# Kernel optimization log

Hardware: AMD Instinct MI355X
Metric: run time of the kernel (lower is better)

The kernel has to match this reference:

```python
import jax, jax.numpy as jnp
import numpy as np

B, N, C = 2, 2048, 1024
H = 16
R = 4
MLP = 4096
LORA_SCALE = 1.0 / R  # lora_alpha=1, r=4
EPS = 1e-5


def _ln(x, g, b):
    m = jnp.mean(x, axis=-1, keepdims=True)
    v = jnp.mean(jnp.square(x - m), axis=-1, keepdims=True)
    return (x - m) * jax.lax.rsqrt(v + EPS) * g + b


def setup_inputs() -> dict:
    key = jax.random.key(0)
    ks = jax.random.split(key, 16)
    s = lambda k, shape, fan: jax.random.normal(k, shape, jnp.float32) * (1.0 / np.sqrt(fan))
    return {
        "x": jax.random.normal(ks[0], (B, N, C), jnp.float32),
        "pos": jax.random.normal(ks[1], (B, N, C), jnp.float32),
        "Wqkv": s(ks[2], (3 * C, C), C),
        "b_qkv": jnp.zeros((3 * C,), jnp.float32),
        "lora_A": s(ks[3], (2 * R, C), C),          # rows 0:R -> q, R:2R -> v
        "lora_B": s(ks[4], (2 * C, R), R) * 0.1,     # rows 0:C -> q, C:2C -> v
        "Wproj": s(ks[5], (C, C), C),
        "b_proj": jnp.zeros((C,), jnp.float32),
        "ln1_g": jnp.ones((C,), jnp.float32),
        "ln1_b": jnp.zeros((C,), jnp.float32),
        "ln2_g": jnp.ones((C,), jnp.float32),
        "ln2_b": jnp.zeros((C,), jnp.float32),
        "W1": s(ks[6], (MLP, C), C),
        "b1": jnp.zeros((MLP,), jnp.float32),
        "W2": s(ks[7], (C, MLP), MLP),
        "b2": jnp.zeros((C,), jnp.float32),
        "idx": 0,
    }


def reference(x, pos, Wqkv, b_qkv, lora_A, lora_B, Wproj, b_proj,
              ln1_g, ln1_b, ln2_g, ln2_b, W1, b1, W2, b2, idx):
    # (dropout layers are identity in eval mode)
    x = x + pos

    # --- attention block: Residual(PreNormDrop(SelfAttention)) ---
    h = _ln(x, ln1_g, ln1_b)                              # [B,N,C]
    qkv = h @ Wqkv.T + b_qkv                              # [B,N,3C]
    # LoRA MergedLinear: low-rank update on q and v thirds only
    after_A = h @ lora_A.T                                # [B,N,2R]
    dq = after_A[..., :R] @ lora_B[:C].T * LORA_SCALE     # [B,N,C]
    dv = after_A[..., R:] @ lora_B[C:].T * LORA_SCALE     # [B,N,C]
    qkv = qkv.at[..., :C].add(dq).at[..., 2 * C:].add(dv)

    Dh = C // H
    q, k, v = [t.reshape(B, N, H, Dh).transpose(0, 2, 1, 3)
               for t in jnp.split(qkv, 3, axis=-1)]       # each [B,H,N,Dh]
    scale = Dh ** -0.5
    attn = jnp.einsum('bhid,bhjd->bhij', q, k) * scale    # [B,H,N,N]
    attn = jax.nn.softmax(attn, axis=-1)
    o = jnp.einsum('bhij,bhjd->bhid', attn, v)            # [B,H,N,Dh]
    o = o.transpose(0, 2, 1, 3).reshape(B, N, C)
    o = o @ Wproj.T + b_proj
    x = x + o

    # --- FFN block: Residual(PreNorm(FeedForward)) ---
    h2 = _ln(x, ln2_g, ln2_b)
    h2 = jax.nn.gelu(h2 @ W1.T + b1, approximate=False)
    h2 = h2 @ W2.T + b2
    return x + h2
```

## Files before the change

### kernel.cpp

```cpp
#include <hip/hip_runtime.h>
#include <hip/hip_bf16.h>
#include <math.h>

typedef __hip_bfloat16 bf16;
typedef __attribute__((ext_vector_type(4))) float f32x4;
typedef __attribute__((ext_vector_type(16))) float f32x16;
typedef __attribute__((ext_vector_type(8))) short s16x8;

__device__ __forceinline__ void async_cp16(void* lds, const void* g) {
    __builtin_amdgcn_global_load_lds((const __attribute__((address_space(1))) void*)g,
                                     (__attribute__((address_space(3))) void*)lds, 16, 0, 0);
}

__device__ __forceinline__ float gelu_fast(float x) {
    float y = 1.5957691216f * (x + 0.044715f * x * x * x);
    float t = __expf(y);
    float th = 1.0f - 2.0f / (t + 1.0f);
    return 0.5f * x * (1.0f + th);
}

__global__ __launch_bounds__(256)
void cvt_all(const float* __restrict__ w0, const float* __restrict__ w1,
             const float* __restrict__ w2, const float* __restrict__ w3,
             bf16* __restrict__ o0, bf16* __restrict__ o1,
             bf16* __restrict__ o2, bf16* __restrict__ o3) {
    int i = blockIdx.x * 256 + threadIdx.x;
    const float* src; bf16* dst; int j = i;
    if (j < 786432)            { src = w0; dst = o0; }
    else if (j < 1048576)      { j -= 786432;  src = w1; dst = o1; }
    else if (j < 2097152)      { j -= 1048576; src = w2; dst = o2; }
    else                       { j -= 2097152; src = w3; dst = o3; }
    float4 v = ((const float4*)src)[j];
    union { bf16 o[4]; uint2 u; } pk;
    pk.o[0] = __float2bfloat16(v.x); pk.o[1] = __float2bfloat16(v.y);
    pk.o[2] = __float2bfloat16(v.z); pk.o[3] = __float2bfloat16(v.w);
    ((uint2*)dst)[j] = pk.u;
}

template <bool ADD>
__global__ __launch_bounds__(256)
void ln_kernel(const float* __restrict__ xin, const float* __restrict__ pos,
               const float* __restrict__ gam, const float* __restrict__ bet,
               float* __restrict__ x1, bf16* __restrict__ hout) {
    const int row = blockIdx.x, tid = threadIdx.x;
    const size_t off = (size_t)row * 1024;
    float4 v = ((const float4*)(xin + off))[tid];
    if constexpr (ADD) {
        float4 p = ((const float4*)(pos + off))[tid];
        v.x += p.x; v.y += p.y; v.z += p.z; v.w += p.w;
        ((float4*)(x1 + off))[tid] = v;
    }
    float s  = v.x + v.y + v.z + v.w;
    float s2 = v.x*v.x + v.y*v.y + v.z*v.z + v.w*v.w;
#pragma unroll
    for (int o = 32; o >= 1; o >>= 1) { s += __shfl_xor(s, o); s2 += __shfl_xor(s2, o); }
    __shared__ float sS[4], sS2[4];
    int w = tid >> 6, lane = tid & 63;
    if (lane == 0) { sS[w] = s; sS2[w] = s2; }
    __syncthreads();
    float mean = (sS[0] + sS[1] + sS[2] + sS[3]) * (1.f / 1024.f);
    float e2   = (sS2[0] + sS2[1] + sS2[2] + sS2[3]) * (1.f / 1024.f);
    float rstd = rsqrtf(e2 - mean * mean + 1e-5f);
    float4 gv = ((const float4*)gam)[tid], bv = ((const float4*)bet)[tid];
    bf16* ho = hout + off + tid * 4;
    ho[0] = __float2bfloat16((v.x - mean) * rstd * gv.x + bv.x);
    ho[1] = __float2bfloat16((v.y - mean) * rstd * gv.y + bv.y);
    ho[2] = __float2bfloat16((v.z - mean) * rstd * gv.z + bv.z);
    ho[3] = __float2bfloat16((v.w - mean) * rstd * gv.w + bv.w);
}

template <int MODE>
__global__ __launch_bounds__(512)
void gemm_bk64(const bf16* __restrict__ A, const bf16* __restrict__ B,
               const float* __restrict__ bias, bf16* __restrict__ outp,
               int M, int N, int K, int gx) {
    __shared__ bf16 As[3][256 * 64];
    __shared__ bf16 Bs[3][128 * 64];
    const int tid = threadIdx.x;
    const int lane = tid & 63, w = tid >> 6;
    const int grp = lane >> 4, c16 = lane & 15;
    const int wm = (w & 3) * 64, wn = (w >> 2) * 64;
    const int nwg = gridDim.x, bid = blockIdx.x;
    const int sw = (bid & 7) * (nwg >> 3) + (bid >> 3);
    const int bm = (sw / gx) * 256, bn = (sw % gx) * 128;

    f32x4 acc[4][4];
    const f32x4 zero = {0.f, 0.f, 0.f, 0.f};
#pragma unroll
    for (int mi = 0; mi < 4; mi++)
#pragma unroll
        for (int ni = 0; ni < 4; ni++) acc[mi][ni] = zero;

#define STAGE128(bufi, k0)                                                          \
    {                                                                               \
        const int buf_ = (bufi);                                                    \
        const int koff_ = (k0);                                                     \
        _Pragma("unroll") for (int t_ = 0; t_ < 4; t_++) {                          \
            int s_ = t_ * 512 + tid;                                                \
            int row_ = s_ >> 3, db_ = s_ & 7;                                       \
            int gb_ = (db_ ^ (row_ & 7)) << 3;                                      \
            async_cp16(&As[buf_][s_ * 8], A + (size_t)(bm + row_) * K + koff_ + gb_); \
        }                                                                           \
        _Pragma("unroll") for (int t_ = 0; t_ < 2; t_++) {                          \
            int s_ = t_ * 512 + tid;                                                \
            int row_ = s_ >> 3, db_ = s_ & 7;                                       \
            int gb_ = (db_ ^ (row_ & 7)) << 3;                                      \
            async_cp16(&Bs[buf_][s_ * 8], B + (size_t)(bn + row_) * K + koff_ + gb_); \
        }                                                                           \
    }

#define COMPUTE128(bufi)                                                            \
    {                                                                               \
        const int buf_ = (bufi);                                                    \
        _Pragma("unroll") for (int kc_ = 0; kc_ < 2; kc_++) {                       \
            s16x8 af_[4], bfv_[4];                                                  \
            _Pragma("unroll") for (int mi_ = 0; mi_ < 4; mi_++) {                   \
                int r_ = wm + mi_ * 16 + c16;                                       \
                af_[mi_] = *(const s16x8*)&As[buf_][r_ * 64 + ((((kc_ << 2) | grp) ^ (r_ & 7)) << 3)]; \
            }                                                                       \
            _Pragma("unroll") for (int ni_ = 0; ni_ < 4; ni_++) {                   \
                int r_ = wn + ni_ * 16 + c16;                                       \
                bfv_[ni_] = *(const s16x8*)&Bs[buf_][r_ * 64 + ((((kc_ << 2) | grp) ^ (r_ & 7)) << 3)]; \
            }                                                                       \
            _Pragma("unroll") for (int mi_ = 0; mi_ < 4; mi_++)                     \
                _Pragma("unroll") for (int ni_ = 0; ni_ < 4; ni_++)                 \
                    acc[mi_][ni_] = __builtin_amdgcn_mfma_f32_16x16x32_bf16(af_[mi_], bfv_[ni_], acc[mi_][ni_], 0, 0, 0); \
        }                                                                           \
    }

#define WAITV12 asm volatile("s_waitcnt vmcnt(12)" ::: "memory")
#define WAITV6  asm volatile("s_waitcnt vmcnt(6)"  ::: "memory")
#define WAITV0  asm volatile("s_waitcnt vmcnt(0)"  ::: "memory")

#define STEP128(BQ, TQ)                                                             \
    {                                                                               \
        const int tq_ = (TQ);                                                       \
        COMPUTE128(BQ);                                                             \
        __builtin_amdgcn_s_barrier();            \
        if (tq_ + 3 < nk) { STAGE128(BQ, (tq_ + 3) << 6); WAITV12; }                 \
        else if (tq_ + 2 < nk) { WAITV6; }                                          \
        else { WAITV0; }                                \
        __builtin_amdgcn_s_barrier();             \
    }

    const int nk = K >> 6;
    STAGE128(0, 0);
    STAGE128(1, 64);
    STAGE128(2, 128);
    WAITV12;
    __builtin_amdgcn_s_barrier();

    for (int t = 0; t < nk - 1; t += 3) {
        STEP128(0, t);
        STEP128(1, t + 1);
        STEP128(2, t + 2);
    }
    COMPUTE128(0);

#undef STEP128
#undef WAITV12
#undef WAITV6
#undef WAITV0
#undef STAGE128
#undef COMPUTE128

#pragma unroll
    for (int mi = 0; mi < 4; mi++)
#pragma unroll
        for (int ni = 0; ni < 4; ni++) {
            int r0 = bm + wm + mi * 16 + grp * 4;
            int c  = bn + wn + ni * 16 + c16;
            float bv = bias[c];
#pragma unroll
            for (int q = 0; q < 4; q++) {
                size_t idx = (size_t)(r0 + q) * N + c;
                float v = acc[mi][ni][q] + bv;
                if constexpr (MODE == 2) v = gelu_fast(v);
                outp[idx] = __float2bfloat16(v);
            }
        }
}

__global__ __launch_bounds__(256)
void gemm_n64(const bf16* __restrict__ A, const bf16* __restrict__ B,
              const float* __restrict__ bias, const float* __restrict__ resid,
              float* __restrict__ outp, int M, int N, int K, int gx) {
    __shared__ bf16 As[3][128 * 64];
    __shared__ bf16 Bs[3][64 * 64];
    const int tid = threadIdx.x;
    const int lane = tid & 63, w = tid >> 6;
    const int grp = lane >> 4, c16 = lane & 15;
    const int wm = w * 32;
    const int nwg = gridDim.x, bid = blockIdx.x;
    const int sw = (bid & 7) * (nwg >> 3) + (bid >> 3);
    const int bm = (sw / gx) * 128, bn = (sw % gx) * 64;

    f32x4 acc[2][4];
    const f32x4 zero = {0.f, 0.f, 0.f, 0.f};
#pragma unroll
    for (int mi = 0; mi < 2; mi++)
#pragma unroll
        for (int ni = 0; ni < 4; ni++) acc[mi][ni] = zero;

#define STAGE64(bufi, k0)                                                           \
    {                                                                               \
        const int buf_ = (bufi);                                                    \
        const int koff_ = (k0);                                                     \
        _Pragma("unroll") for (int t_ = 0; t_ < 4; t_++) {                          \
            int s_ = t_ * 256 + tid;                                                \
            int row_ = s_ >> 3, db_ = s_ & 7;                                       \
            async_cp16(&As[buf_][s_ * 8], A + (size_t)(bm + row_) * K + koff_ + ((db_ ^ (row_ & 7)) << 3)); \
        }                                                                           \
        _Pragma("unroll") for (int t_ = 0; t_ < 2; t_++) {                          \
            int s_ = t_ * 256 + tid;                                                \
            int row_ = s_ >> 3, db_ = s_ & 7;                                       \
            async_cp16(&Bs[buf_][s_ * 8], B + (size_t)(bn + row_) * K + koff_ + ((db_ ^ (row_ & 7)) << 3)); \
        }                                                                           \
    }

#define COMPUTE64(bufi)                                                             \
    {                                                                               \
        const int buf_ = (bufi);                                                    \
        _Pragma("unroll") for (int kc_ = 0; kc_ < 2; kc_++) {                       \
            s16x8 af_[2], bfv_[4];                                                  \
            _Pragma("unroll") for (int mi_ = 0; mi_ < 2; mi_++) {                   \
                int r_ = wm + mi_ * 16 + c16;                                       \
                af_[mi_] = *(const s16x8*)&As[buf_][r_ * 64 + ((((kc_ << 2) | grp) ^ (r_ & 7)) << 3)]; \
            }                                                                       \
            _Pragma("unroll") for (int ni_ = 0; ni_ < 4; ni_++) {                   \
                int rb_ = ni_ * 16 + c16;                                           \
                bfv_[ni_] = *(const s16x8*)&Bs[buf_][rb_ * 64 + ((((kc_ << 2) | grp) ^ (rb_ & 7)) << 3)]; \
            }                                                                       \
            _Pragma("unroll") for (int mi_ = 0; mi_ < 2; mi_++)                     \
                _Pragma("unroll") for (int ni_ = 0; ni_ < 4; ni_++)                 \
                    acc[mi_][ni_] = __builtin_amdgcn_mfma_f32_16x16x32_bf16(af_[mi_], bfv_[ni_], acc[mi_][ni_], 0, 0, 0); \
        }                                                                           \
    }

#define WAITV12 asm volatile("s_waitcnt vmcnt(12)" ::: "memory")
#define WAITV6  asm volatile("s_waitcnt vmcnt(6)"  ::: "memory")
#define WAITV0  asm volatile("s_waitcnt vmcnt(0)"  ::: "memory")

#define STEP64(BQ, TQ)                                                              \
    {                                                                               \
        const int tq_ = (TQ);                                                       \
        COMPUTE64(BQ);                                                              \
        __builtin_amdgcn_s_barrier();            \
        if (tq_ + 3 < nk) { STAGE64(BQ, (tq_ + 3) << 6); WAITV12; }                 \
        else if (tq_ + 2 < nk) { WAITV6; }                                          \
        else { WAITV0; }                                \
        __builtin_amdgcn_s_barrier();             \
    }

    const int nk = K >> 6;
    STAGE64(0, 0);
    STAGE64(1, 64);
    STAGE64(2, 128);
    WAITV12;
    __builtin_amdgcn_s_barrier();

    for (int t = 0; t < nk - 1; t += 3) {
        STEP64(0, t);
        STEP64(1, t + 1);
        STEP64(2, t + 2);
    }
    COMPUTE64(0);

#undef STEP64
#undef WAITV12
#undef WAITV6
#undef WAITV0
#undef STAGE64
#undef COMPUTE64

#pragma unroll
    for (int mi = 0; mi < 2; mi++)
#pragma unroll
        for (int ni = 0; ni < 4; ni++) {
            int r0 = bm + wm + mi * 16 + grp * 4;
            int c  = bn + ni * 16 + c16;
            float bv = bias[c];
#pragma unroll
            for (int q = 0; q < 4; q++) {
                size_t idx = (size_t)(r0 + q) * N + c;
                outp[idx] = acc[mi][ni][q] + bv + resid[idx];
            }
        }
}

__global__ __launch_bounds__(256)
void lora_a_kernel(const bf16* __restrict__ h, const float* __restrict__ A,
                   float* __restrict__ afterA) {
    const int row = blockIdx.x, tid = threadIdx.x;
    float hv[4];
#pragma unroll
    for (int t = 0; t < 4; t++) hv[t] = __bfloat162float(h[(size_t)row * 1024 + tid * 4 + t]);
    float p[8];
#pragma unroll
    for (int r = 0; r < 8; r++) {
        float4 av = ((const float4*)(A + (size_t)r * 1024))[tid];
        p[r] = hv[0] * av.x + hv[1] * av.y + hv[2] * av.z + hv[3] * av.w;
    }
#pragma unroll
    for (int r = 0; r < 8; r++)
#pragma unroll
        for (int o = 32; o >= 1; o >>= 1) p[r] += __shfl_xor(p[r], o);
    __shared__ float red[4][8];
    int w = tid >> 6, lane = tid & 63;
    if (lane == 0) {
#pragma unroll
        for (int r = 0; r < 8; r++) red[w][r] = p[r];
    }
    __syncthreads();
    if (tid < 8) afterA[(size_t)row * 8 + tid] = red[0][tid] + red[1][tid] + red[2][tid] + red[3][tid];
}

__global__ __launch_bounds__(256)
void attn_prep(const bf16* __restrict__ qkv, const float* __restrict__ afterA,
               const float* __restrict__ loraB, bf16* __restrict__ Qb,
               bf16* __restrict__ Kb, bf16* __restrict__ Vt) {
    const int bh = blockIdx.y, b = bh >> 4, h = bh & 15;
    const int it = blockIdx.x;
    __shared__ bf16 Vs[64 * 65];
    const int tid = threadIdx.x;
#pragma unroll
    for (int t = 0; t < 16; t++) {
        int s = t * 256 + tid;
        int il = s >> 6, d = s & 63;
        int ig = b * 2048 + it * 64 + il;
        size_t grow = (size_t)ig * 3072 + h * 64 + d;
        int col = h * 64 + d;
        const float* aA = afterA + (size_t)ig * 8;
        float4 bq = ((const float4*)loraB)[col];
        float4 bvv = ((const float4*)loraB)[1024 + col];
        float dq = (aA[0]*bq.x  + aA[1]*bq.y  + aA[2]*bq.z  + aA[3]*bq.w)  * 0.25f;
        float dv = (aA[4]*bvv.x + aA[5]*bvv.y + aA[6]*bvv.z + aA[7]*bvv.w) * 0.25f;
        float q = (__bfloat162float(qkv[grow]) + dq) * 0.18033688011f;
        float k = __bfloat162float(qkv[grow + 1024]);
        float v = __bfloat162float(qkv[grow + 2048]) + dv;
        size_t orow = (size_t)(bh * 2048 + it * 64 + il) * 64 + d;
        Qb[orow] = __float2bfloat16(q);
        Kb[orow] = __float2bfloat16(k);
        Vs[d * 65 + il] = __float2bfloat16(v);
    }
    __syncthreads();
#pragma unroll
    for (int t = 0; t < 16; t++) {
        int s = t * 256 + tid;
        int d = s >> 6, il = s & 63;
        Vt[(size_t)(bh * 64 + d) * 2048 + it * 64 + il] = Vs[d * 65 + il];
    }
}

__global__ __launch_bounds__(256)
void attn_fused(const bf16* __restrict__ Qb, const bf16* __restrict__ Kb,
                const bf16* __restrict__ Vt, bf16* __restrict__ Og) {
    __shared__ bf16 Qs[128 * 64], Ks[2][64 * 64], Vs[2][64 * 64];
    const int tid = threadIdx.x;
    const int lane = tid & 63, w = tid >> 6;
    const int c32 = lane & 31, l5 = lane >> 5;
    const int bid = blockIdx.x;
    const int sw = (bid & 7) * 64 + (bid >> 3);
    const int bh = sw >> 4, b = bh >> 4, h = bh & 15;
    const int i0 = (sw & 15) * 128;
    const int rowperm = (c32 & 19) | (((c32 >> 3) & 1) << 2) | (((c32 >> 2) & 1) << 3);

    const size_t qbase = (size_t)(bh * 2048 + i0) * 64;
    const size_t kbase = (size_t)bh * 2048 * 64;
    const size_t vbase = (size_t)bh * 64 * 2048;

#define STAGEKV(bufi, jv)                                                           \
    {                                                                               \
        const int buf_ = (bufi);                                                    \
        const int joff_ = (jv);                                                     \
        _Pragma("unroll") for (int t_ = 0; t_ < 2; t_++) {                          \
            int s_ = t_ * 256 + tid;                                                \
            int row_ = s_ >> 3, db_ = s_ & 7;                                       \
            int gb_ = (db_ ^ (row_ & 7)) << 3;                                      \
            async_cp16(&Ks[buf_][s_ * 8], Kb + kbase + (size_t)(joff_ + row_) * 64 + gb_); \
            async_cp16(&Vs[buf_][s_ * 8], Vt + vbase + (size_t)row_ * 2048 + joff_ + gb_); \
        }                                                                           \
    }

#pragma unroll
    for (int t = 0; t < 4; t++) {
        int s = t * 256 + tid;
        int row = s >> 3, db = s & 7;
        async_cp16(&Qs[s * 8], Qb + qbase + row * 64 + ((db ^ (row & 7)) << 3));
    }
    STAGEKV(0, 0);
    __syncthreads();

    s16x8 qf[4];
    {
        int rq = w * 32 + c32;
#pragma unroll
        for (int kc = 0; kc < 4; kc++) {
            int db = 2 * kc + l5;
            qf[kc] = *(const s16x8*)&Qs[rq * 64 + ((db ^ (rq & 7)) << 3)];
        }
    }

    f32x16 Oq[2];
#pragma unroll
    for (int dq = 0; dq < 2; dq++)
#pragma unroll
        for (int r = 0; r < 16; r++) Oq[dq][r] = 0.f;
    float l_lane = 0.f;

#define ATILE(BUF, JN)                                                              \
    {                                                                               \
        const int jn_ = (JN);                                                       \
        if (jn_ < 32) { STAGEKV((BUF) ^ 1, jn_ << 6); }                             \
        f32x16 Sq[2];                                                               \
        __builtin_amdgcn_s_setprio(1);                                              \
        _Pragma("unroll") for (int jq_ = 0; jq_ < 2; jq_++) {                       \
            _Pragma("unroll") for (int r_ = 0; r_ < 16; r_++) Sq[jq_][r_] = 0.f;    \
            int rk_ = jq_ * 32 + rowperm;                                           \
            _Pragma("unroll") for (int kc_ = 0; kc_ < 4; kc_++) {                   \
                int db_ = 2 * kc_ + l5;                                             \
                s16x8 af_ = *(const s16x8*)&Ks[BUF][rk_ * 64 + ((db_ ^ (rk_ & 7)) << 3)]; \
                Sq[jq_] = __builtin_amdgcn_mfma_f32_32x32x16_bf16(af_, qf[kc_], Sq[jq_], 0, 0, 0); \
            }                                                                       \
        }                                                                           \
        __builtin_amdgcn_s_setprio(0);                                              \
        s16x8 pf_[4];                                                               \
        _Pragma("unroll") for (int kc_ = 0; kc_ < 4; kc_++) {                       \
            union { s16x8 v; unsigned u4[4]; } u_;                                  \
            _Pragma("unroll") for (int pr_ = 0; pr_ < 4; pr_++) {                   \
                float a_ = Sq[kc_ >> 1][8 * (kc_ & 1) + 2 * pr_];                   \
                float b_ = Sq[kc_ >> 1][8 * (kc_ & 1) + 2 * pr_ + 1];               \
                float pa_, pb_;                                                     \
                asm("v_exp_f32 %0, %1" : "=v"(pa_) : "v"(a_));                      \
                asm("v_exp_f32 %0, %1" : "=v"(pb_) : "v"(b_));                      \
                l_lane += pa_; l_lane += pb_;                                       \
                unsigned pk_;                                                       \
                asm("v_cvt_pk_bf16_f32 %0, %1, %2" : "=v"(pk_) : "v"(pa_), "v"(pb_)); \
                u_.u4[pr_] = pk_;                                                   \
            }                                                                       \
            pf_[kc_] = u_.v;                                                        \
        }                                                                           \
        __builtin_amdgcn_s_setprio(1);                                              \
        _Pragma("unroll") for (int dq_ = 0; dq_ < 2; dq_++) {                       \
            int rd_ = dq_ * 32 + c32;                                               \
            _Pragma("unroll") for (int kc_ = 0; kc_ < 4; kc_++) {                   \
                int jb_ = 2 * kc_ + l5;                                             \
                s16x8 af_ = *(const s16x8*)&Vs[BUF][rd_ * 64 + ((jb_ ^ (rd_ & 7)) << 3)]; \
                Oq[dq_] = __builtin_amdgcn_mfma_f32_32x32x16_bf16(af_, pf_[kc_], Oq[dq_], 0, 0, 0); \
            }                                                                       \
        }                                                                           \
        __builtin_amdgcn_s_setprio(0);                                              \
        __syncthreads();                                                            \
    }

    for (int jt = 0; jt < 32; jt += 2) {
        ATILE(0, jt + 1);
        ATILE(1, jt + 2);
    }
#undef ATILE
#undef STAGEKV

    float l = l_lane + __shfl_xor(l_lane, 32);
    float inv = 1.0f / fmaxf(l, 1e-35f);
    int i = i0 + w * 32 + c32;
    size_t obase = (size_t)(b * 2048 + i) * 1024 + h * 64;
#pragma unroll
    for (int dq = 0; dq < 2; dq++)
#pragma unroll
        for (int rg = 0; rg < 4; rg++) {
            union { bf16 e[4]; uint2 u; } pk;
#pragma unroll
            for (int c = 0; c < 4; c++)
                pk.e[c] = __float2bfloat16(Oq[dq][rg * 4 + c] * inv);
            int d0 = dq * 32 + l5 * 4 + rg * 8;
            *(uint2*)&Og[obase + d0] = pk.u;
        }
}

extern "C" void kernel_launch(void* const* d_in, const int* in_sizes, int n_in,
                              void* d_out, int out_size, void* d_ws, size_t ws_size,
                              hipStream_t stream) {
    const float* x     = (const float*)d_in[0];
    const float* pos   = (const float*)d_in[1];
    const float* Wqkv  = (const float*)d_in[2];
    const float* bqkv  = (const float*)d_in[3];
    const float* loraA = (const float*)d_in[4];
    const float* loraB = (const float*)d_in[5];
    const float* Wproj = (const float*)d_in[6];
    const float* bproj = (const float*)d_in[7];
    const float* ln1g  = (const float*)d_in[8];
    const float* ln1b  = (const float*)d_in[9];
    const float* ln2g  = (const float*)d_in[10];
    const float* ln2b  = (const float*)d_in[11];
    const float* W1    = (const float*)d_in[12];
    const float* b1    = (const float*)d_in[13];
    const float* W2    = (const float*)d_in[14];
    const float* b2    = (const float*)d_in[15];

    char* ws = (char*)d_ws;
    float* x1     = (float*)(ws + 0);
    bf16*  hbuf   = (bf16*) (ws + 16777216);
    bf16*  qkv    = (bf16*) (ws + 25165824);
    bf16*  gbuf   = (bf16*) (ws + 50331648);
    float* afterA = (float*)(ws + 83886080);
    bf16*  Qb     = (bf16*) (ws + 84017152);
    bf16*  Kb     = (bf16*) (ws + 92405760);
    bf16*  Vt     = (bf16*) (ws + 100794368);
    bf16*  Obf    = (bf16*) (ws + 109182976);
    bf16*  Wqkvb  = (bf16*) (ws + 117571584);
    bf16*  Wprojb = (bf16*) (ws + 123863040);
    bf16*  W1b    = (bf16*) (ws + 125960192);
    bf16*  W2b    = (bf16*) (ws + 134348800);

    cvt_all<<<12288, 256, 0, stream>>>(Wqkv, Wproj, W1, W2, Wqkvb, Wprojb, W1b, W2b);

    ln_kernel<true><<<4096, 256, 0, stream>>>(x, pos, ln1g, ln1b, x1, hbuf);

    gemm_bk64<0><<<384, 512, 0, stream>>>(hbuf, Wqkvb, bqkv, qkv, 4096, 3072, 1024, 24);

    lora_a_kernel<<<4096, 256, 0, stream>>>(hbuf, loraA, afterA);

    attn_prep<<<dim3(32, 32), 256, 0, stream>>>(qkv, afterA, loraB, Qb, Kb, Vt);
    attn_fused<<<512, 256, 0, stream>>>(Qb, Kb, Vt, Obf);

    gemm_n64<<<512, 256, 0, stream>>>(Obf, Wprojb, bproj, x1, x1, 4096, 1024, 1024, 16);

    ln_kernel<false><<<4096, 256, 0, stream>>>(x1, nullptr, ln2g, ln2b, nullptr, hbuf);

    gemm_bk64<2><<<512, 512, 0, stream>>>(hbuf, W1b, b1, gbuf, 4096, 4096, 1024, 32);

    gemm_n64<<<512, 256, 0, stream>>>(gbuf, W2b, b2, x1, (float*)d_out, 4096, 1024, 4096, 16);

    (void)in_sizes; (void)n_in; (void)out_size; (void)ws_size;
}
```

Before: 381.7 us.

## Enlarge per-warp GEMM tiles and halve threads per block

The 256x128 GEMM now runs with 4 warps instead of 8, so each warp computes a 128x64 sub-tile with 32 accumulators. The N=1024 GEMMs move from 128x64 to 128x128 block tiles, with each warp computing 64x64. Both changes raise MFMA work per LDS fragment load and cut block count. The cost is higher register pressure, fewer waves per CU for latency hiding, and for the N=1024 GEMMs only 256 blocks, which may underfill the CUs.

```diff
diff --git a/kernel.cpp b/kernel.cpp
--- a/kernel.cpp
+++ b/kernel.cpp
@@ -70,7 +70,7 @@
 }
 
 template <int MODE>
-__global__ __launch_bounds__(512)
+__global__ __launch_bounds__(256, 1)
 void gemm_bk64(const bf16* __restrict__ A, const bf16* __restrict__ B,
                const float* __restrict__ bias, bf16* __restrict__ outp,
                int M, int N, int K, int gx) {
@@ -79,15 +79,15 @@
     const int tid = threadIdx.x;
     const int lane = tid & 63, w = tid >> 6;
     const int grp = lane >> 4, c16 = lane & 15;
-    const int wm = (w & 3) * 64, wn = (w >> 2) * 64;
+    const int wm = (w & 1) * 128, wn = (w >> 1) * 64;
     const int nwg = gridDim.x, bid = blockIdx.x;
     const int sw = (bid & 7) * (nwg >> 3) + (bid >> 3);
     const int bm = (sw / gx) * 256, bn = (sw % gx) * 128;
 
-    f32x4 acc[4][4];
+    f32x4 acc[8][4];
     const f32x4 zero = {0.f, 0.f, 0.f, 0.f};
 #pragma unroll
-    for (int mi = 0; mi < 4; mi++)
+    for (int mi = 0; mi < 8; mi++)
 #pragma unroll
         for (int ni = 0; ni < 4; ni++) acc[mi][ni] = zero;
 
@@ -95,14 +95,14 @@
     {                                                                               \
         const int buf_ = (bufi);                                                    \
         const int koff_ = (k0);                                                     \
-        _Pragma("unroll") for (int t_ = 0; t_ < 4; t_++) {                          \
-            int s_ = t_ * 512 + tid;                                                \
+        _Pragma("unroll") for (int t_ = 0; t_ < 8; t_++) {                          \
+            int s_ = t_ * 256 + tid;                                                \
             int row_ = s_ >> 3, db_ = s_ & 7;                                       \
             int gb_ = (db_ ^ (row_ & 7)) << 3;                                      \
             async_cp16(&As[buf_][s_ * 8], A + (size_t)(bm + row_) * K + koff_ + gb_); \
         }                                                                           \
-        _Pragma("unroll") for (int t_ = 0; t_ < 2; t_++) {                          \
-            int s_ = t_ * 512 + tid;                                                \
+        _Pragma("unroll") for (int t_ = 0; t_ < 4; t_++) {                          \
+            int s_ = t_ * 256 + tid;                                                \
             int row_ = s_ >> 3, db_ = s_ & 7;                                       \
             int gb_ = (db_ ^ (row_ & 7)) << 3;                                      \
             async_cp16(&Bs[buf_][s_ * 8], B + (size_t)(bn + row_) * K + koff_ + gb_); \
@@ -113,8 +113,8 @@
     {                                                                               \
         const int buf_ = (bufi);                                                    \
         _Pragma("unroll") for (int kc_ = 0; kc_ < 2; kc_++) {                       \
-            s16x8 af_[4], bfv_[4];                                                  \
-            _Pragma("unroll") for (int mi_ = 0; mi_ < 4; mi_++) {                   \
+            s16x8 af_[8], bfv_[4];                                                  \
+            _Pragma("unroll") for (int mi_ = 0; mi_ < 8; mi_++) {                   \
                 int r_ = wm + mi_ * 16 + c16;                                       \
                 af_[mi_] = *(const s16x8*)&As[buf_][r_ * 64 + ((((kc_ << 2) | grp) ^ (r_ & 7)) << 3)]; \
             }                                                                       \
@@ -122,14 +122,14 @@
                 int r_ = wn + ni_ * 16 + c16;                                       \
                 bfv_[ni_] = *(const s16x8*)&Bs[buf_][r_ * 64 + ((((kc_ << 2) | grp) ^ (r_ & 7)) << 3)]; \
             }                                                                       \
-            _Pragma("unroll") for (int mi_ = 0; mi_ < 4; mi_++)                     \
+            _Pragma("unroll") for (int mi_ = 0; mi_ < 8; mi_++)                     \
                 _Pragma("unroll") for (int ni_ = 0; ni_ < 4; ni_++)                 \
                     acc[mi_][ni_] = __builtin_amdgcn_mfma_f32_16x16x32_bf16(af_[mi_], bfv_[ni_], acc[mi_][ni_], 0, 0, 0); \
         }                                                                           \
     }
 
+#define WAITV24 asm volatile("s_waitcnt vmcnt(24)" ::: "memory")
 #define WAITV12 asm volatile("s_waitcnt vmcnt(12)" ::: "memory")
-#define WAITV6  asm volatile("s_waitcnt vmcnt(6)"  ::: "memory")
 #define WAITV0  asm volatile("s_waitcnt vmcnt(0)"  ::: "memory")
 
 #define STEP128(BQ, TQ)                                                             \
@@ -137,8 +137,8 @@
         const int tq_ = (TQ);                                                       \
         COMPUTE128(BQ);                                                             \
         __builtin_amdgcn_s_barrier();            \
-        if (tq_ + 3 < nk) { STAGE128(BQ, (tq_ + 3) << 6); WAITV12; }                 \
-        else if (tq_ + 2 < nk) { WAITV6; }                                          \
+        if (tq_ + 3 < nk) { STAGE128(BQ, (tq_ + 3) << 6); WAITV24; }                \
+        else if (tq_ + 2 < nk) { WAITV12; }                                         \
         else { WAITV0; }                                \
         __builtin_amdgcn_s_barrier();             \
     }
@@ -147,7 +147,7 @@
     STAGE128(0, 0);
     STAGE128(1, 64);
     STAGE128(2, 128);
-    WAITV12;
+    WAITV24;
     __builtin_amdgcn_s_barrier();
 
     for (int t = 0; t < nk - 1; t += 3) {
@@ -158,14 +158,14 @@
     COMPUTE128(0);
 
 #undef STEP128
+#undef WAITV24
 #undef WAITV12
-#undef WAITV6
 #undef WAITV0
 #undef STAGE128
 #undef COMPUTE128
 
 #pragma unroll
-    for (int mi = 0; mi < 4; mi++)
+    for (int mi = 0; mi < 8; mi++)
 #pragma unroll
         for (int ni = 0; ni < 4; ni++) {
             int r0 = bm + wm + mi * 16 + grp * 4;
@@ -181,24 +181,24 @@
         }
 }
 
-__global__ __launch_bounds__(256)
+__global__ __launch_bounds__(256, 1)
 void gemm_n64(const bf16* __restrict__ A, const bf16* __restrict__ B,
               const float* __restrict__ bias, const float* __restrict__ resid,
               float* __restrict__ outp, int M, int N, int K, int gx) {
     __shared__ bf16 As[3][128 * 64];
-    __shared__ bf16 Bs[3][64 * 64];
+    __shared__ bf16 Bs[3][128 * 64];
     const int tid = threadIdx.x;
     const int lane = tid & 63, w = tid >> 6;
     const int grp = lane >> 4, c16 = lane & 15;
-    const int wm = w * 32;
+    const int wm = (w & 1) * 64, wn = (w >> 1) * 64;
     const int nwg = gridDim.x, bid = blockIdx.x;
     const int sw = (bid & 7) * (nwg >> 3) + (bid >> 3);
-    const int bm = (sw / gx) * 128, bn = (sw % gx) * 64;
-
-    f32x4 acc[2][4];
+    const int bm = (sw / gx) * 128, bn = (sw % gx) * 128;
+
+    f32x4 acc[4][4];
     const f32x4 zero = {0.f, 0.f, 0.f, 0.f};
 #pragma unroll
-    for (int mi = 0; mi < 2; mi++)
+    for (int mi = 0; mi < 4; mi++)
 #pragma unroll
         for (int ni = 0; ni < 4; ni++) acc[mi][ni] = zero;
 
@@ -209,12 +209,9 @@
         _Pragma("unroll") for (int t_ = 0; t_ < 4; t_++) {                          \
             int s_ = t_ * 256 + tid;                                                \
             int row_ = s_ >> 3, db_ = s_ & 7;                                       \
-            async_cp16(&As[buf_][s_ * 8], A + (size_t)(bm + row_) * K + koff_ + ((db_ ^ (row_ & 7)) << 3)); \
-        }                                                                           \
-        _Pragma("unroll") for (int t_ = 0; t_ < 2; t_++) {                          \
-            int s_ = t_ * 256 + tid;                                                \
-            int row_ = s_ >> 3, db_ = s_ & 7;                                       \
-            async_cp16(&Bs[buf_][s_ * 8], B + (size_t)(bn + row_) * K + koff_ + ((db_ ^ (row_ & 7)) << 3)); \
+            int gb_ = (db_ ^ (row_ & 7)) << 3;                                      \
+            async_cp16(&As[buf_][s_ * 8], A + (size_t)(bm + row_) * K + koff_ + gb_); \
+            async_cp16(&Bs[buf_][s_ * 8], B + (size_t)(bn + row_) * K + koff_ + gb_); \
         }                                                                           \
     }
 
@@ -222,23 +219,23 @@
     {                                                                               \
         const int buf_ = (bufi);                                                    \
         _Pragma("unroll") for (int kc_ = 0; kc_ < 2; kc_++) {                       \
-            s16x8 af_[2], bfv_[4];                                                  \
-            _Pragma("unroll") for (int mi_ = 0; mi_ < 2; mi_++) {                   \
+            s16x8 af_[4], bfv_[4];                                                  \
+            _Pragma("unroll") for (int mi_ = 0; mi_ < 4; mi_++) {                   \
                 int r_ = wm + mi_ * 16 + c16;                                       \
                 af_[mi_] = *(const s16x8*)&As[buf_][r_ * 64 + ((((kc_ << 2) | grp) ^ (r_ & 7)) << 3)]; \
             }                                                                       \
             _Pragma("unroll") for (int ni_ = 0; ni_ < 4; ni_++) {                   \
-                int rb_ = ni_ * 16 + c16;                                           \
-                bfv_[ni_] = *(const s16x8*)&Bs[buf_][rb_ * 64 + ((((kc_ << 2) | grp) ^ (rb_ & 7)) << 3)]; \
-            }                                                                       \
-            _Pragma("unroll") for (int mi_ = 0; mi_ < 2; mi_++)                     \
+                int r_ = wn + ni_ * 16 + c16;                                       \
+                bfv_[ni_] = *(const s16x8*)&Bs[buf_][r_ * 64 + ((((kc_ << 2) | grp) ^ (r_ & 7)) << 3)]; \
+            }                                                                       \
+            _Pragma("unroll") for (int mi_ = 0; mi_ < 4; mi_++)                     \
                 _Pragma("unroll") for (int ni_ = 0; ni_ < 4; ni_++)                 \
                     acc[mi_][ni_] = __builtin_amdgcn_mfma_f32_16x16x32_bf16(af_[mi_], bfv_[ni_], acc[mi_][ni_], 0, 0, 0); \
         }                                                                           \
     }
 
-#define WAITV12 asm volatile("s_waitcnt vmcnt(12)" ::: "memory")
-#define WAITV6  asm volatile("s_waitcnt vmcnt(6)"  ::: "memory")
+#define WAITV16 asm volatile("s_waitcnt vmcnt(16)" ::: "memory")
+#define WAITV8  asm volatile("s_waitcnt vmcnt(8)"  ::: "memory")
 #define WAITV0  asm volatile("s_waitcnt vmcnt(0)"  ::: "memory")
 
 #define STEP64(BQ, TQ)                                                              \
@@ -246,8 +243,8 @@
         const int tq_ = (TQ);                                                       \
         COMPUTE64(BQ);                                                              \
         __builtin_amdgcn_s_barrier();            \
-        if (tq_ + 3 < nk) { STAGE64(BQ, (tq_ + 3) << 6); WAITV12; }                 \
-        else if (tq_ + 2 < nk) { WAITV6; }                                          \
+        if (tq_ + 3 < nk) { STAGE64(BQ, (tq_ + 3) << 6); WAITV16; }                 \
+        else if (tq_ + 2 < nk) { WAITV8; }                                          \
         else { WAITV0; }                                \
         __builtin_amdgcn_s_barrier();             \
     }
@@ -256,7 +253,7 @@
     STAGE64(0, 0);
     STAGE64(1, 64);
     STAGE64(2, 128);
-    WAITV12;
+    WAITV16;
     __builtin_amdgcn_s_barrier();
 
     for (int t = 0; t < nk - 1; t += 3) {
@@ -267,18 +264,18 @@
     COMPUTE64(0);
 
 #undef STEP64
-#undef WAITV12
-#undef WAITV6
+#undef WAITV16
+#undef WAITV8
 #undef WAITV0
 #undef STAGE64
 #undef COMPUTE64
 
 #pragma unroll
-    for (int mi = 0; mi < 2; mi++)
+    for (int mi = 0; mi < 4; mi++)
 #pragma unroll
         for (int ni = 0; ni < 4; ni++) {
             int r0 = bm + wm + mi * 16 + grp * 4;
-            int c  = bn + ni * 16 + c16;
+            int c  = bn + wn + ni * 16 + c16;
             float bv = bias[c];
 #pragma unroll
             for (int q = 0; q < 4; q++) {
@@ -516,20 +513,20 @@
 
     ln_kernel<true><<<4096, 256, 0, stream>>>(x, pos, ln1g, ln1b, x1, hbuf);
 
-    gemm_bk64<0><<<384, 512, 0, stream>>>(hbuf, Wqkvb, bqkv, qkv, 4096, 3072, 1024, 24);
+    gemm_bk64<0><<<384, 256, 0, stream>>>(hbuf, Wqkvb, bqkv, qkv, 4096, 3072, 1024, 24);
 
     lora_a_kernel<<<4096, 256, 0, stream>>>(hbuf, loraA, afterA);
 
     attn_prep<<<dim3(32, 32), 256, 0, stream>>>(qkv, afterA, loraB, Qb, Kb, Vt);
     attn_fused<<<512, 256, 0, stream>>>(Qb, Kb, Vt, Obf);
 
-    gemm_n64<<<512, 256, 0, stream>>>(Obf, Wprojb, bproj, x1, x1, 4096, 1024, 1024, 16);
+    gemm_n64<<<256, 256, 0, stream>>>(Obf, Wprojb, bproj, x1, x1, 4096, 1024, 1024, 8);
 
     ln_kernel<false><<<4096, 256, 0, stream>>>(x1, nullptr, ln2g, ln2b, nullptr, hbuf);
 
-    gemm_bk64<2><<<512, 512, 0, stream>>>(hbuf, W1b, b1, gbuf, 4096, 4096, 1024, 32);
-
-    gemm_n64<<<512, 256, 0, stream>>>(gbuf, W2b, b2, x1, (float*)d_out, 4096, 1024, 4096, 16);
+    gemm_bk64<2><<<512, 256, 0, stream>>>(hbuf, W1b, b1, gbuf, 4096, 4096, 1024, 32);
+
+    gemm_n64<<<256, 256, 0, stream>>>(gbuf, W2b, b2, x1, (float*)d_out, 4096, 1024, 4096, 8);
 
     (void)in_sizes; (void)n_in; (void)out_size; (void)ws_size;
 }
```

After: 401.4 us. 1.05x slower.
